# Performance work log

Measured on AMD Instinct MI355X. Metric: run time of the kernel, lower is better.

The kernel has to match this reference:

```python
import jax, jax.numpy as jnp
import numpy as np
import math

B, T, C = 4, 2048, 1024
NH = 16
HD = C // NH


def setup_inputs() -> dict:
    key = jax.random.key(0)
    ks = jax.random.split(key, 10)
    s = 0.02
    x = jax.random.normal(ks[0], (B, T, C), dtype=jnp.float32)
    W_qkv = jax.random.normal(ks[1], (C, 3 * C), dtype=jnp.float32) * s
    b_qkv = jnp.zeros((3 * C,), dtype=jnp.float32)
    W_proj = jax.random.normal(ks[2], (C, C), dtype=jnp.float32) * s
    b_proj = jnp.zeros((C,), dtype=jnp.float32)
    asym_mean, asym_std = 1.0, 0.7
    q_scale = jax.random.normal(ks[3], (NH, HD), dtype=jnp.float32) * asym_std + asym_mean
    q_bias = jax.random.normal(ks[4], (NH, HD), dtype=jnp.float32) * asym_std + asym_mean
    k_scale = jax.random.normal(ks[5], (NH, HD), dtype=jnp.float32) * asym_std + asym_mean
    k_bias = jax.random.normal(ks[6], (NH, HD), dtype=jnp.float32) * asym_std + asym_mean
    return {"x": x, "W_qkv": W_qkv, "b_qkv": b_qkv, "W_proj": W_proj,
            "b_proj": b_proj, "q_scale": q_scale, "q_bias": q_bias,
            "k_scale": k_scale, "k_bias": k_bias}


def reference(x, W_qkv, b_qkv, W_proj, b_proj, q_scale, q_bias, k_scale, k_bias):
    Bx, Tx, Cx = x.shape
    qkv = x @ W_qkv + b_qkv                       # [B,T,3C]
    q, k, v = jnp.split(qkv, 3, axis=-1)
    # [B,T,C] -> [B,NH,T,HD]
    reshape = lambda t: t.reshape(Bx, Tx, NH, HD).transpose(0, 2, 1, 3)
    q, k, v = reshape(q), reshape(k), reshape(v)
    # per-head affine scaling of Q/K
    q = q * q_scale[None, :, None, :] + q_bias[None, :, None, :]
    k = k * k_scale[None, :, None, :] + k_bias[None, :, None, :]
    scores = jnp.einsum('bhqd,bhkd->bhqk', q, k) / math.sqrt(HD)  # [B,NH,T,T]
    causal = jnp.tril(jnp.ones((Tx, Tx), dtype=bool))
    scores = jnp.where(causal[None, None], scores, -jnp.inf)
    att = jax.nn.softmax(scores, axis=-1)
    y = jnp.einsum('bhqk,bhkd->bhqd', att, v)     # [B,NH,T,HD]
    y = y.transpose(0, 2, 1, 3).reshape(Bx, Tx, Cx)
    return y @ W_proj + b_proj
```

## Files before the change

kernel.cpp:

```cpp
#include <hip/hip_runtime.h>
#include <hip/hip_bf16.h>

typedef unsigned short u16;
typedef __attribute__((ext_vector_type(8))) short short8;
typedef __attribute__((ext_vector_type(4))) float floatx4;

#define B_SZ 4
#define T_SZ 2048
#define C_SZ 1024
#define NH_SZ 16
#define HD_SZ 64
#define M_TOT 8192
#define K_DIM 1024

#define QSCALE 0.1803368801111204f

#define OFF_XB   ((size_t)16)
#define OFF_WQT  (OFF_XB + 8388608)
#define OFF_WPT  (OFF_WQT + 3145728)
#define OFF_PB   (OFF_WPT + 1048576)
#define OFF_Q    (OFF_PB + 8192)
#define OFF_K    (OFF_Q + 8388608)
#define OFF_V    (OFF_K + 8388608)
#define OFF_Y    (OFF_V + 8388608)
#define PB_BQKV  0
#define PB_BPROJ 3072
#define PB_QSC   4096
#define PB_QBI   5120
#define PB_KSC   6144
#define PB_KBI   7168

__device__ __forceinline__ float bf2f(u16 u) {
    return __uint_as_float(((unsigned)u) << 16);
}
__device__ __forceinline__ u16 f2bf(float f) {
    unsigned x = __float_as_uint(f);
    unsigned r = (x + 0x7fffu + ((x >> 16) & 1u)) >> 16;
    return (u16)r;
}
__device__ __forceinline__ u16 f2bf_fast(float f) {
    return (u16)((__float_as_uint(f) + 0x8000u) >> 16);
}
__device__ __forceinline__ void gl_lds16(const u16* g, u16* l) {
    __builtin_amdgcn_global_load_lds(
        (const __attribute__((address_space(1))) void*)g,
        (__attribute__((address_space(3))) void*)l, 16, 0, 0);
}
__device__ __forceinline__ int detect_isf(const u16* xx, int lane) {
    float v0 = fabsf(bf2f(xx[lane * 2]));
    float v1 = fabsf(bf2f(xx[lane * 2 + 1]));
    int b0 = (v0 > 1024.0f) || (v0 != 0.0f && v0 < 9.5367431640625e-7f);
    int b1 = (v1 > 1024.0f) || (v1 != 0.0f && v1 < 9.5367431640625e-7f);
    unsigned long long ba = __ballot(b0), bb = __ballot(b1);
    return (__popcll(ba) + __popcll(bb)) > 8;
}

__global__ __launch_bounds__(256) void prep_k(
        const void* __restrict__ x,
        const void* __restrict__ Wqkv, const void* __restrict__ Wproj,
        const void* __restrict__ bqkv, const void* __restrict__ bproj,
        const void* __restrict__ qsc, const void* __restrict__ qbi,
        const void* __restrict__ ksc, const void* __restrict__ kbi,
        u16* __restrict__ xb, u16* __restrict__ Wt_qkv,
        u16* __restrict__ Wt_proj, u16* __restrict__ pb,
        int* __restrict__ flag) {
    __shared__ u16 t[32][33];
    const int blk = blockIdx.x;
    const int isf = detect_isf((const u16*)x, threadIdx.x & 63);
    if (blk == 0 && threadIdx.x == 0) flag[0] = isf;
    if (blk < 8192) {
        const int i = blk * 256 + threadIdx.x;
        if (isf) {
            const float4 v = ((const float4*)x)[i];
            ushort4 o;
            o.x = f2bf(v.x); o.y = f2bf(v.y); o.z = f2bf(v.z); o.w = f2bf(v.w);
            ((ushort4*)xb)[i] = o;
        } else {
            ((ushort4*)xb)[i] = ((const ushort4*)x)[i];
        }
        return;
    }
    if (blk < 8200) {
        const int i4 = (blk - 8192) * 256 + threadIdx.x;
        if (i4 >= 2048) return;
        const int e = i4 * 4;
        const void* src; int off;
        if (e < 3072)      { src = bqkv;  off = e; }
        else if (e < 4096) { src = bproj; off = e - 3072; }
        else if (e < 5120) { src = qsc;   off = e - 4096; }
        else if (e < 6144) { src = qbi;   off = e - 5120; }
        else if (e < 7168) { src = ksc;   off = e - 6144; }
        else               { src = kbi;   off = e - 7168; }
        ushort4 o;
        if (isf) {
            const float4 v = *(const float4*)((const float*)src + off);
            o.x = f2bf(v.x); o.y = f2bf(v.y); o.z = f2bf(v.z); o.w = f2bf(v.w);
        } else {
            o = *(const ushort4*)((const u16*)src + off);
        }
        *(ushort4*)&pb[e] = o;
        return;
    }
    const void* in; u16* out; int R, C, idx;
    if (blk < 11272) { idx = blk - 8200;  in = Wqkv;  out = Wt_qkv;  R = 1024; C = 3072; }
    else             { idx = blk - 11272; in = Wproj; out = Wt_proj; R = 1024; C = 1024; }
    const int nbx = C >> 5;
    const int c0 = (idx % nbx) * 32, r0 = (idx / nbx) * 32;
    const int tx = threadIdx.x & 31, ty = threadIdx.x >> 5;
    for (int i = 0; i < 4; i++) {
        int r = ty + i * 8;
        size_t gi = (size_t)(r0 + r) * C + c0 + tx;
        t[r][tx] = isf ? f2bf(((const float*)in)[gi]) : ((const u16*)in)[gi];
    }
    __syncthreads();
    for (int i = 0; i < 4; i++) {
        int cr = ty + i * 8;
        out[(size_t)(c0 + cr) * R + r0 + tx] = t[tx][cr];
    }
}

#define QG_BM 256
#define QG_BN 192
#define QG_NT 16

__global__ __launch_bounds__(512, 2) void qkv_gemm(
        const u16* __restrict__ X, const u16* __restrict__ Wt,
        const u16* __restrict__ pb,
        u16* __restrict__ Qb, u16* __restrict__ Kb, u16* __restrict__ Vb) {
    __shared__ __align__(16) u16 As[2][QG_BM * 64];
    __shared__ __align__(16) u16 Bs[2][QG_BN * 64];
    const int bm = blockIdx.y * QG_BM, bn = blockIdx.x * QG_BN;
    const int tid = threadIdx.x;
    const int lane = tid & 63, w = tid >> 6;
    const int quad = lane >> 4, l16 = lane & 15;
    const int wm = (w >> 2) * 128;
    const int wn = (w & 3) * 48;
    const int lrow = lane >> 3;
    const int lcol = ((lane & 7) ^ lrow) * 8;
    const int sl0 = ((0 + quad) ^ (l16 & 7)) * 8;
    const int sl1 = ((4 + quad) ^ (l16 & 7)) * 8;

#define QG_STAGE(slot, kt) do {                                                  \
        const int k0_ = (kt) * 64;                                               \
        _Pragma("unroll")                                                        \
        for (int j = 0; j < 4; j++) {                                            \
            const int rb = w * 32 + j * 8;                                       \
            gl_lds16(&X[(size_t)(bm + rb + lrow) * K_DIM + k0_ + lcol],          \
                     &As[slot][rb * 64]);                                        \
        }                                                                        \
        _Pragma("unroll")                                                        \
        for (int j = 0; j < 3; j++) {                                            \
            const int rb = w * 24 + j * 8;                                       \
            gl_lds16(&Wt[(size_t)(bn + rb + lrow) * K_DIM + k0_ + lcol],         \
                     &Bs[slot][rb * 64]);                                        \
        }                                                                        \
    } while (0)

    floatx4 acc[8][3];
#pragma unroll
    for (int mi = 0; mi < 8; mi++)
#pragma unroll
        for (int ni = 0; ni < 3; ni++) acc[mi][ni] = 0.f;

    QG_STAGE(0, 0);
    QG_STAGE(1, 1);
    asm volatile("s_waitcnt vmcnt(7)" ::: "memory");
    __builtin_amdgcn_s_barrier();

    for (int t = 0; t < QG_NT; ++t) {
        const int cur = t & 1;
        const u16* as = As[cur];
        const u16* bs = Bs[cur];
        short8 a[8], b[3];
#pragma unroll
        for (int mi = 0; mi < 8; mi++)
            a[mi] = *(const short8*)&as[(wm + mi * 16 + l16) * 64 + sl0];
#pragma unroll
        for (int ni = 0; ni < 3; ni++)
            b[ni] = *(const short8*)&bs[(wn + ni * 16 + l16) * 64 + sl0];
        __builtin_amdgcn_s_setprio(1);
#pragma unroll
        for (int mi = 0; mi < 8; mi++)
#pragma unroll
            for (int ni = 0; ni < 3; ni++)
                acc[mi][ni] = __builtin_amdgcn_mfma_f32_16x16x32_bf16(
                    a[mi], b[ni], acc[mi][ni], 0, 0, 0);
        __builtin_amdgcn_s_setprio(0);
#pragma unroll
        for (int mi = 0; mi < 8; mi++)
            a[mi] = *(const short8*)&as[(wm + mi * 16 + l16) * 64 + sl1];
#pragma unroll
        for (int ni = 0; ni < 3; ni++)
            b[ni] = *(const short8*)&bs[(wn + ni * 16 + l16) * 64 + sl1];
        asm volatile("s_waitcnt lgkmcnt(0)" ::: "memory");
        __builtin_amdgcn_s_barrier();
        if (t < QG_NT - 1) {
            const int tn = (t + 2 < QG_NT) ? t + 2 : QG_NT - 1;
            QG_STAGE(cur, tn);
        }
        __builtin_amdgcn_s_setprio(1);
#pragma unroll
        for (int mi = 0; mi < 8; mi++)
#pragma unroll
            for (int ni = 0; ni < 3; ni++)
                acc[mi][ni] = __builtin_amdgcn_mfma_f32_16x16x32_bf16(
                    a[mi], b[ni], acc[mi][ni], 0, 0, 0);
        __builtin_amdgcn_s_setprio(0);
        asm volatile("s_waitcnt vmcnt(7)" ::: "memory");
        __builtin_amdgcn_s_barrier();
    }
#undef QG_STAGE

    const int bb = bm >> 11;
    const int tbase = bm & 2047;
#pragma unroll
    for (int ni = 0; ni < 3; ni++) {
        const int col = bn + wn + ni * 16 + l16;
        const int sec = col >> 10;
        const int cmod = col & 1023;
        const int h = cmod >> 6, d = cmod & 63;
        const float bv = bf2f(pb[PB_BQKV + col]);
        if (sec == 2) {
#pragma unroll
            for (int mi = 0; mi < 8; mi++) {
                const int t0 = tbase + wm + mi * 16 + quad * 4;
                ushort4 pk;
                pk.x = f2bf(acc[mi][ni][0] + bv);
                pk.y = f2bf(acc[mi][ni][1] + bv);
                pk.z = f2bf(acc[mi][ni][2] + bv);
                pk.w = f2bf(acc[mi][ni][3] + bv);
                *(ushort4*)&Vb[(((size_t)(bb * NH_SZ + h)) * HD_SZ + d) * T_SZ + t0] = pk;
            }
        } else {
            float sA, sB;
            if (sec == 0) {
                sA = bf2f(pb[PB_QSC + h * 64 + d]) * QSCALE;
                sB = bf2f(pb[PB_QBI + h * 64 + d]) * QSCALE;
            } else {
                sA = bf2f(pb[PB_KSC + h * 64 + d]);
                sB = bf2f(pb[PB_KBI + h * 64 + d]);
            }
            u16* dstbuf = (sec == 0) ? Qb : Kb;
#pragma unroll
            for (int mi = 0; mi < 8; mi++)
#pragma unroll
                for (int r = 0; r < 4; r++) {
                    const int tt = tbase + wm + mi * 16 + quad * 4 + r;
                    float v = (acc[mi][ni][r] + bv) * sA + sB;
                    dstbuf[(((size_t)(bb * NH_SZ + h)) * T_SZ + tt) * HD_SZ + d] = f2bf(v);
                }
        }
    }
}

__global__ __launch_bounds__(512) void attn_k(const u16* __restrict__ Qb,
                                              const u16* __restrict__ Kb,
                                              const u16* __restrict__ Vtg,
                                              u16* __restrict__ Y) {
    __shared__ __align__(16) u16 Ks[64 * 64];
    __shared__ __align__(16) u16 Vs[64 * 64];
    __shared__ __align__(16) u16 Ps[8 * 16 * 88];
    const int blk = blockIdx.x;
    const int head = blk & 63;
    const int p = blk >> 6;
    const int b = head >> 4, h = head & 15;
    const int tid = threadIdx.x, lane = tid & 63, w = tid >> 6;
    const int quad = lane >> 4, l16 = lane & 15;
    const size_t qk_off = (size_t)head * (T_SZ * HD_SZ);
    const size_t v_off = (size_t)head * (HD_SZ * T_SZ);
    u16* psw = &Ps[w * 1408];
    const int lr = lane >> 3;
    const int lc = ((lane & 7) ^ lr) * 8;
    const int sl0 = ((quad) ^ (l16 & 7)) * 8;
    const int sl1 = ((4 + quad) ^ (l16 & 7)) * 8;

    short8 ones;
    for (int j = 0; j < 8; j++) ones[j] = (short)0x3F80;

    for (int tile = 0; tile < 2; tile++) {
        const int qt = tile ? p : (15 - p);
        const int q0 = qt * 128;
        const int rbase = q0 + w * 16;
        const int q = rbase + l16;

        const short8 aq0 = *(const short8*)&Qb[qk_off + (size_t)q * HD_SZ + quad * 8];
        const short8 aq1 = *(const short8*)&Qb[qk_off + (size_t)q * HD_SZ + 32 + quad * 8];

        floatx4 o[4];
        for (int mi = 0; mi < 4; mi++) o[mi] = 0.f;
        float m_run = -1e30f, l_run = 0.f;

        for (int k0 = 0; k0 < q0 + 128; k0 += 64) {
            __syncthreads();
            gl_lds16(&Kb[qk_off + (size_t)(k0 + w * 8 + lr) * HD_SZ + lc], &Ks[w * 512]);
            gl_lds16(&Vtg[v_off + (size_t)(w * 8 + lr) * T_SZ + k0 + lc], &Vs[w * 512]);
            __syncthreads();
            if (k0 > rbase + 15) continue;

            floatx4 s[4];
            for (int ni = 0; ni < 4; ni++) s[ni] = 0.f;
            for (int ni = 0; ni < 4; ni++)
                s[ni] = __builtin_amdgcn_mfma_f32_16x16x32_bf16(
                    *(const short8*)&Ks[(ni * 16 + l16) * 64 + sl0], aq0, s[ni], 0, 0, 0);
            for (int ni = 0; ni < 4; ni++)
                s[ni] = __builtin_amdgcn_mfma_f32_16x16x32_bf16(
                    *(const short8*)&Ks[(ni * 16 + l16) * 64 + sl1], aq1, s[ni], 0, 0, 0);

            if (k0 + 63 > rbase) {
                for (int ni = 0; ni < 4; ni++)
                    for (int r = 0; r < 4; r++) {
                        int key = k0 + ni * 16 + quad * 4 + r;
                        if (key > q) s[ni][r] = -1e30f;
                    }
            }

            float mx = fmaxf(fmaxf(s[0][0], s[0][1]), fmaxf(s[0][2], s[0][3]));
            for (int ni = 1; ni < 4; ni++)
                mx = fmaxf(mx, fmaxf(fmaxf(s[ni][0], s[ni][1]),
                                     fmaxf(s[ni][2], s[ni][3])));
            mx = fmaxf(mx, __shfl_xor(mx, 16, 64));
            mx = fmaxf(mx, __shfl_xor(mx, 32, 64));
            const float mnew = fmaxf(m_run, mx);
            const float alpha = exp2f(m_run - mnew);
            for (int ni = 0; ni < 4; ni++)
                for (int r = 0; r < 4; r++)
                    s[ni][r] = exp2f(s[ni][r] - mnew);
            m_run = mnew;
            for (int mi = 0; mi < 4; mi++) o[mi] *= alpha;

            for (int ni = 0; ni < 4; ni++) {
                ushort4 pk;
                pk.x = f2bf_fast(s[ni][0]); pk.y = f2bf_fast(s[ni][1]);
                pk.z = f2bf_fast(s[ni][2]); pk.w = f2bf_fast(s[ni][3]);
                *(ushort4*)&psw[l16 * 88 + ni * 16 + quad * 4] = pk;
            }

            floatx4 s4 = 0.f;
            for (int kk = 0; kk < 64; kk += 32) {
                short8 pfr = *(const short8*)&psw[l16 * 88 + kk + quad * 8];
                const int vsl = (kk == 0) ? sl0 : sl1;
                s4 = __builtin_amdgcn_mfma_f32_16x16x32_bf16(ones, pfr, s4, 0, 0, 0);
                for (int mi = 0; mi < 4; mi++) {
                    short8 vfr = *(const short8*)&Vs[(mi * 16 + l16) * 64 + vsl];
                    o[mi] = __builtin_amdgcn_mfma_f32_16x16x32_bf16(vfr, pfr, o[mi], 0, 0, 0);
                }
            }
            l_run = l_run * alpha + s4[0];
        }

        const float inv = 1.0f / l_run;
        u16* yrow = &Y[(((size_t)b * T_SZ + q) * NH_SZ + h) * HD_SZ];
        for (int mi = 0; mi < 4; mi++) {
            ushort4 pk;
            pk.x = f2bf_fast(o[mi][0] * inv); pk.y = f2bf_fast(o[mi][1] * inv);
            pk.z = f2bf_fast(o[mi][2] * inv); pk.w = f2bf_fast(o[mi][3] * inv);
            *(ushort4*)&yrow[mi * 16 + quad * 4] = pk;
        }
    }
}

__global__ __launch_bounds__(256) void proj_gemm(const u16* __restrict__ Yin,
                                                 const u16* __restrict__ Wt,
                                                 const u16* __restrict__ pb,
                                                 void* __restrict__ out,
                                                 const int* __restrict__ flag) {
    __shared__ __align__(16) u16 As[128 * 64];
    __shared__ __align__(16) u16 Bs[128 * 64];
    const int isf = flag[0];
    const int bm = blockIdx.y * 128, bn = blockIdx.x * 128;
    const int tid = threadIdx.x;
    const int lane = tid & 63, wave = tid >> 6;
    const int quad = lane >> 4, l16 = lane & 15;
    const int wm = (wave & 1) * 64, wn = (wave >> 1) * 64;
    const int lrow = lane >> 3;
    const int lcol = ((lane & 7) ^ lrow) * 8;

    floatx4 acc[4][4];
    for (int mi = 0; mi < 4; mi++)
        for (int ni = 0; ni < 4; ni++) acc[mi][ni] = 0.f;

    for (int k0 = 0; k0 < K_DIM; k0 += 64) {
        __syncthreads();
        for (int j = 0; j < 4; j++) {
            const int rb = wave * 32 + j * 8;
            gl_lds16(&Yin[(size_t)(bm + rb + lrow) * K_DIM + k0 + lcol], &As[rb * 64]);
            gl_lds16(&Wt[(size_t)(bn + rb + lrow) * K_DIM + k0 + lcol], &Bs[rb * 64]);
        }
        __syncthreads();
        for (int kk = 0; kk < 64; kk += 32) {
            const int cb = kk >> 3;
            const int slot = ((cb + quad) ^ (l16 & 7)) * 8;
            short8 a[4], b[4];
            for (int mi = 0; mi < 4; mi++)
                a[mi] = *(const short8*)&As[(wm + mi * 16 + l16) * 64 + slot];
            for (int ni = 0; ni < 4; ni++)
                b[ni] = *(const short8*)&Bs[(wn + ni * 16 + l16) * 64 + slot];
            for (int mi = 0; mi < 4; mi++)
                for (int ni = 0; ni < 4; ni++)
                    acc[mi][ni] = __builtin_amdgcn_mfma_f32_16x16x32_bf16(
                        a[mi], b[ni], acc[mi][ni], 0, 0, 0);
        }
    }

    for (int mi = 0; mi < 4; mi++) {
        for (int ni = 0; ni < 4; ni++) {
            const int col = bn + wn + ni * 16 + l16;
            const float bv = bf2f(pb[PB_BPROJ + col]);
            for (int r = 0; r < 4; r++) {
                const int row = bm + wm + mi * 16 + quad * 4 + r;
                const float v = acc[mi][ni][r] + bv;
                if (isf) ((float*)out)[(size_t)row * C_SZ + col] = v;
                else     ((u16*)out)[(size_t)row * C_SZ + col] = f2bf(v);
            }
        }
    }
}

extern "C" void kernel_launch(void* const* d_in, const int* in_sizes, int n_in,
                              void* d_out, int out_size, void* d_ws, size_t ws_size,
                              hipStream_t stream) {
    const void* x     = d_in[0];
    const void* Wqkv  = d_in[1];
    const void* bqkv  = d_in[2];
    const void* Wproj = d_in[3];
    const void* bproj = d_in[4];
    const void* qsc   = d_in[5];
    const void* qbi   = d_in[6];
    const void* ksc   = d_in[7];
    const void* kbi   = d_in[8];

    u16* ws = (u16*)d_ws;
    int* flag    = (int*)d_ws;
    u16* xb      = ws + OFF_XB;
    u16* Wt_qkv  = ws + OFF_WQT;
    u16* Wt_proj = ws + OFF_WPT;
    u16* pb      = ws + OFF_PB;
    u16* Qb      = ws + OFF_Q;
    u16* Kb      = ws + OFF_K;
    u16* Vb      = ws + OFF_V;
    u16* Yb      = ws + OFF_Y;

    prep_k<<<12296, 256, 0, stream>>>(x, Wqkv, Wproj, bqkv, bproj,
                                      qsc, qbi, ksc, kbi,
                                      xb, Wt_qkv, Wt_proj, pb, flag);
    qkv_gemm<<<dim3(16, 32), 512, 0, stream>>>(xb, Wt_qkv, pb, Qb, Kb, Vb);
    attn_k<<<dim3(512), 512, 0, stream>>>(Qb, Kb, Vb, Yb);
    proj_gemm<<<dim3(8, 64), 256, 0, stream>>>(Yb, Wt_proj, pb, d_out, flag);
}
```

Baseline: 297.5 us.

## Double-buffer K/V and projection GEMM tiles with async loads, lazy softmax rescale

Attention now double-buffers the K/V tiles in LDS. The next tile's global-to-LDS load is issued before computing on the current one, using explicit vmcnt waits and barriers instead of two __syncthreads per step. The online softmax skips rescaling of the output and running sum unless the running max grows by more than 8 (in log2 units), and packs bf16 with v_cvt_pk_bf16_f32. The projection GEMM gets a two-stage LDS pipeline that prefetches k-tile t+2 while computing, plus s_setprio around MFMA bursts and launch bounds of 2 blocks per SM. The costs are doubled LDS use, which may lower occupancy, and more fragile hand-written waitcnt logic; the lazy rescale lets unnormalised exponentials grow up to 2^8.

```diff
diff --git a/kernel.cpp b/kernel.cpp
--- a/kernel.cpp
+++ b/kernel.cpp
@@ -40,6 +40,11 @@
 }
 __device__ __forceinline__ u16 f2bf_fast(float f) {
     return (u16)((__float_as_uint(f) + 0x8000u) >> 16);
+}
+__device__ __forceinline__ unsigned cvt_pk_bf16(float lo, float hi) {
+    unsigned r;
+    asm("v_cvt_pk_bf16_f32 %0, %1, %2" : "=v"(r) : "v"(lo), "v"(hi));
+    return r;
 }
 __device__ __forceinline__ void gl_lds16(const u16* g, u16* l) {
     __builtin_amdgcn_global_load_lds(
@@ -257,8 +262,8 @@
                                               const u16* __restrict__ Kb,
                                               const u16* __restrict__ Vtg,
                                               u16* __restrict__ Y) {
-    __shared__ __align__(16) u16 Ks[64 * 64];
-    __shared__ __align__(16) u16 Vs[64 * 64];
+    __shared__ __align__(16) u16 Ks[2][64 * 64];
+    __shared__ __align__(16) u16 Vs[2][64 * 64];
     __shared__ __align__(16) u16 Ps[8 * 16 * 88];
     const int blk = blockIdx.x;
     const int head = blk & 63;
@@ -282,6 +287,7 @@
         const int q0 = qt * 128;
         const int rbase = q0 + w * 16;
         const int q = rbase + l16;
+        const int nt = (q0 >> 6) + 2;
 
         const short8 aq0 = *(const short8*)&Qb[qk_off + (size_t)q * HD_SZ + quad * 8];
         const short8 aq1 = *(const short8*)&Qb[qk_off + (size_t)q * HD_SZ + 32 + quad * 8];
@@ -290,117 +296,185 @@
         for (int mi = 0; mi < 4; mi++) o[mi] = 0.f;
         float m_run = -1e30f, l_run = 0.f;
 
-        for (int k0 = 0; k0 < q0 + 128; k0 += 64) {
-            __syncthreads();
-            gl_lds16(&Kb[qk_off + (size_t)(k0 + w * 8 + lr) * HD_SZ + lc], &Ks[w * 512]);
-            gl_lds16(&Vtg[v_off + (size_t)(w * 8 + lr) * T_SZ + k0 + lc], &Vs[w * 512]);
-            __syncthreads();
-            if (k0 > rbase + 15) continue;
-
-            floatx4 s[4];
-            for (int ni = 0; ni < 4; ni++) s[ni] = 0.f;
-            for (int ni = 0; ni < 4; ni++)
-                s[ni] = __builtin_amdgcn_mfma_f32_16x16x32_bf16(
-                    *(const short8*)&Ks[(ni * 16 + l16) * 64 + sl0], aq0, s[ni], 0, 0, 0);
-            for (int ni = 0; ni < 4; ni++)
-                s[ni] = __builtin_amdgcn_mfma_f32_16x16x32_bf16(
-                    *(const short8*)&Ks[(ni * 16 + l16) * 64 + sl1], aq1, s[ni], 0, 0, 0);
-
-            if (k0 + 63 > rbase) {
+        gl_lds16(&Kb[qk_off + (size_t)(w * 8 + lr) * HD_SZ + lc], &Ks[0][w * 512]);
+        gl_lds16(&Vtg[v_off + (size_t)(w * 8 + lr) * T_SZ + lc], &Vs[0][w * 512]);
+
+        for (int t = 0; t < nt; ++t) {
+            const int cur = t & 1;
+            const int k0 = t * 64;
+            if (t + 1 < nt) {
+                const int kn = k0 + 64;
+                gl_lds16(&Kb[qk_off + (size_t)(kn + w * 8 + lr) * HD_SZ + lc],
+                         &Ks[cur ^ 1][w * 512]);
+                gl_lds16(&Vtg[v_off + (size_t)(w * 8 + lr) * T_SZ + kn + lc],
+                         &Vs[cur ^ 1][w * 512]);
+                asm volatile("s_waitcnt vmcnt(2)" ::: "memory");
+            } else {
+                asm volatile("s_waitcnt vmcnt(0)" ::: "memory");
+            }
+            __builtin_amdgcn_s_barrier();
+
+            if (k0 <= rbase + 15) {
+                const u16* ks = Ks[cur];
+                const u16* vs = Vs[cur];
+                floatx4 s[4];
+                for (int ni = 0; ni < 4; ni++) s[ni] = 0.f;
                 for (int ni = 0; ni < 4; ni++)
-                    for (int r = 0; r < 4; r++) {
-                        int key = k0 + ni * 16 + quad * 4 + r;
-                        if (key > q) s[ni][r] = -1e30f;
+                    s[ni] = __builtin_amdgcn_mfma_f32_16x16x32_bf16(
+                        *(const short8*)&ks[(ni * 16 + l16) * 64 + sl0], aq0, s[ni], 0, 0, 0);
+                for (int ni = 0; ni < 4; ni++)
+                    s[ni] = __builtin_amdgcn_mfma_f32_16x16x32_bf16(
+                        *(const short8*)&ks[(ni * 16 + l16) * 64 + sl1], aq1, s[ni], 0, 0, 0);
+
+                if (k0 + 63 > rbase) {
+                    for (int ni = 0; ni < 4; ni++)
+                        for (int r = 0; r < 4; r++) {
+                            int key = k0 + ni * 16 + quad * 4 + r;
+                            if (key > q) s[ni][r] = -1e30f;
+                        }
+                }
+
+                float t0 = fmaxf(fmaxf(s[0][0], s[0][1]), s[0][2]);
+                float t1 = fmaxf(fmaxf(s[0][3], s[1][0]), s[1][1]);
+                float t2 = fmaxf(fmaxf(s[1][2], s[1][3]), s[2][0]);
+                float t3 = fmaxf(fmaxf(s[2][1], s[2][2]), s[2][3]);
+                float t4 = fmaxf(fmaxf(s[3][0], s[3][1]), s[3][2]);
+                float mx = fmaxf(fmaxf(fmaxf(t0, t1), fmaxf(t2, t3)),
+                                 fmaxf(t4, s[3][3]));
+                mx = fmaxf(mx, __shfl_xor(mx, 16, 64));
+                mx = fmaxf(mx, __shfl_xor(mx, 32, 64));
+
+                if (!__all(mx <= m_run + 8.0f)) {
+                    const float mnew = fmaxf(m_run, mx);
+                    const float alpha = exp2f(m_run - mnew);
+                    m_run = mnew;
+                    for (int mi = 0; mi < 4; mi++) o[mi] *= alpha;
+                    l_run *= alpha;
+                }
+                for (int ni = 0; ni < 4; ni++)
+                    for (int r = 0; r < 4; r++)
+                        s[ni][r] = exp2f(s[ni][r] - m_run);
+
+                for (int ni = 0; ni < 4; ni++) {
+                    uint2 pp;
+                    pp.x = cvt_pk_bf16(s[ni][0], s[ni][1]);
+                    pp.y = cvt_pk_bf16(s[ni][2], s[ni][3]);
+                    *(uint2*)&psw[l16 * 88 + ni * 16 + quad * 4] = pp;
+                }
+
+                floatx4 s4 = 0.f;
+                for (int kk = 0; kk < 64; kk += 32) {
+                    short8 pfr = *(const short8*)&psw[l16 * 88 + kk + quad * 8];
+                    const int vsl = (kk == 0) ? sl0 : sl1;
+                    s4 = __builtin_amdgcn_mfma_f32_16x16x32_bf16(ones, pfr, s4, 0, 0, 0);
+                    for (int mi = 0; mi < 4; mi++) {
+                        short8 vfr = *(const short8*)&vs[(mi * 16 + l16) * 64 + vsl];
+                        o[mi] = __builtin_amdgcn_mfma_f32_16x16x32_bf16(vfr, pfr, o[mi], 0, 0, 0);
                     }
+                }
+                l_run += s4[0];
             }
-
-            float mx = fmaxf(fmaxf(s[0][0], s[0][1]), fmaxf(s[0][2], s[0][3]));
-            for (int ni = 1; ni < 4; ni++)
-                mx = fmaxf(mx, fmaxf(fmaxf(s[ni][0], s[ni][1]),
-                                     fmaxf(s[ni][2], s[ni][3])));
-            mx = fmaxf(mx, __shfl_xor(mx, 16, 64));
-            mx = fmaxf(mx, __shfl_xor(mx, 32, 64));
-            const float mnew = fmaxf(m_run, mx);
-            const float alpha = exp2f(m_run - mnew);
-            for (int ni = 0; ni < 4; ni++)
-                for (int r = 0; r < 4; r++)
-                    s[ni][r] = exp2f(s[ni][r] - mnew);
-            m_run = mnew;
-            for (int mi = 0; mi < 4; mi++) o[mi] *= alpha;
-
-            for (int ni = 0; ni < 4; ni++) {
-                ushort4 pk;
-                pk.x = f2bf_fast(s[ni][0]); pk.y = f2bf_fast(s[ni][1]);
-                pk.z = f2bf_fast(s[ni][2]); pk.w = f2bf_fast(s[ni][3]);
-                *(ushort4*)&psw[l16 * 88 + ni * 16 + quad * 4] = pk;
-            }
-
-            floatx4 s4 = 0.f;
-            for (int kk = 0; kk < 64; kk += 32) {
-                short8 pfr = *(const short8*)&psw[l16 * 88 + kk + quad * 8];
-                const int vsl = (kk == 0) ? sl0 : sl1;
-                s4 = __builtin_amdgcn_mfma_f32_16x16x32_bf16(ones, pfr, s4, 0, 0, 0);
-                for (int mi = 0; mi < 4; mi++) {
-                    short8 vfr = *(const short8*)&Vs[(mi * 16 + l16) * 64 + vsl];
-                    o[mi] = __builtin_amdgcn_mfma_f32_16x16x32_bf16(vfr, pfr, o[mi], 0, 0, 0);
-                }
-            }
-            l_run = l_run * alpha + s4[0];
+            asm volatile("s_waitcnt lgkmcnt(0)" ::: "memory");
+            __builtin_amdgcn_s_barrier();
         }
 
         const float inv = 1.0f / l_run;
         u16* yrow = &Y[(((size_t)b * T_SZ + q) * NH_SZ + h) * HD_SZ];
         for (int mi = 0; mi < 4; mi++) {
-            ushort4 pk;
-            pk.x = f2bf_fast(o[mi][0] * inv); pk.y = f2bf_fast(o[mi][1] * inv);
-            pk.z = f2bf_fast(o[mi][2] * inv); pk.w = f2bf_fast(o[mi][3] * inv);
-            *(ushort4*)&yrow[mi * 16 + quad * 4] = pk;
-        }
-    }
-}
-
-__global__ __launch_bounds__(256) void proj_gemm(const u16* __restrict__ Yin,
-                                                 const u16* __restrict__ Wt,
-                                                 const u16* __restrict__ pb,
-                                                 void* __restrict__ out,
-                                                 const int* __restrict__ flag) {
-    __shared__ __align__(16) u16 As[128 * 64];
-    __shared__ __align__(16) u16 Bs[128 * 64];
+            uint2 pk2;
+            pk2.x = cvt_pk_bf16(o[mi][0] * inv, o[mi][1] * inv);
+            pk2.y = cvt_pk_bf16(o[mi][2] * inv, o[mi][3] * inv);
+            *(uint2*)&yrow[mi * 16 + quad * 4] = pk2;
+        }
+    }
+}
+
+#define PG_NT 16
+
+__global__ __launch_bounds__(256, 2) void proj_gemm(const u16* __restrict__ Yin,
+                                                    const u16* __restrict__ Wt,
+                                                    const u16* __restrict__ pb,
+                                                    void* __restrict__ out,
+                                                    const int* __restrict__ flag) {
+    __shared__ __align__(16) u16 As[2][128 * 64];
+    __shared__ __align__(16) u16 Bs[2][128 * 64];
     const int isf = flag[0];
     const int bm = blockIdx.y * 128, bn = blockIdx.x * 128;
     const int tid = threadIdx.x;
-    const int lane = tid & 63, wave = tid >> 6;
+    const int lane = tid & 63, w = tid >> 6;
     const int quad = lane >> 4, l16 = lane & 15;
-    const int wm = (wave & 1) * 64, wn = (wave >> 1) * 64;
+    const int wm = (w & 1) * 64, wn = (w >> 1) * 64;
     const int lrow = lane >> 3;
     const int lcol = ((lane & 7) ^ lrow) * 8;
+    const int sl0 = ((0 + quad) ^ (l16 & 7)) * 8;
+    const int sl1 = ((4 + quad) ^ (l16 & 7)) * 8;
+
+#define PG_STAGE(slot, kt) do {                                                  \
+        const int k0_ = (kt) * 64;                                               \
+        _Pragma("unroll")                                                        \
+        for (int j = 0; j < 4; j++) {                                            \
+            const int rb = w * 32 + j * 8;                                       \
+            gl_lds16(&Yin[(size_t)(bm + rb + lrow) * K_DIM + k0_ + lcol],        \
+                     &As[slot][rb * 64]);                                        \
+            gl_lds16(&Wt[(size_t)(bn + rb + lrow) * K_DIM + k0_ + lcol],         \
+                     &Bs[slot][rb * 64]);                                        \
+        }                                                                        \
+    } while (0)
 
     floatx4 acc[4][4];
+#pragma unroll
     for (int mi = 0; mi < 4; mi++)
+#pragma unroll
         for (int ni = 0; ni < 4; ni++) acc[mi][ni] = 0.f;
 
-    for (int k0 = 0; k0 < K_DIM; k0 += 64) {
-        __syncthreads();
-        for (int j = 0; j < 4; j++) {
-            const int rb = wave * 32 + j * 8;
-            gl_lds16(&Yin[(size_t)(bm + rb + lrow) * K_DIM + k0 + lcol], &As[rb * 64]);
-            gl_lds16(&Wt[(size_t)(bn + rb + lrow) * K_DIM + k0 + lcol], &Bs[rb * 64]);
-        }
-        __syncthreads();
-        for (int kk = 0; kk < 64; kk += 32) {
-            const int cb = kk >> 3;
-            const int slot = ((cb + quad) ^ (l16 & 7)) * 8;
-            short8 a[4], b[4];
-            for (int mi = 0; mi < 4; mi++)
-                a[mi] = *(const short8*)&As[(wm + mi * 16 + l16) * 64 + slot];
+    PG_STAGE(0, 0);
+    PG_STAGE(1, 1);
+    asm volatile("s_waitcnt vmcnt(8)" ::: "memory");
+    __builtin_amdgcn_s_barrier();
+
+    for (int t = 0; t < PG_NT; ++t) {
+        const int cur = t & 1;
+        const u16* as = As[cur];
+        const u16* bs = Bs[cur];
+        short8 a[4], b[4];
+#pragma unroll
+        for (int mi = 0; mi < 4; mi++)
+            a[mi] = *(const short8*)&as[(wm + mi * 16 + l16) * 64 + sl0];
+#pragma unroll
+        for (int ni = 0; ni < 4; ni++)
+            b[ni] = *(const short8*)&bs[(wn + ni * 16 + l16) * 64 + sl0];
+        __builtin_amdgcn_s_setprio(1);
+#pragma unroll
+        for (int mi = 0; mi < 4; mi++)
+#pragma unroll
             for (int ni = 0; ni < 4; ni++)
-                b[ni] = *(const short8*)&Bs[(wn + ni * 16 + l16) * 64 + slot];
-            for (int mi = 0; mi < 4; mi++)
-                for (int ni = 0; ni < 4; ni++)
-                    acc[mi][ni] = __builtin_amdgcn_mfma_f32_16x16x32_bf16(
-                        a[mi], b[ni], acc[mi][ni], 0, 0, 0);
-        }
-    }
+                acc[mi][ni] = __builtin_amdgcn_mfma_f32_16x16x32_bf16(
+                    a[mi], b[ni], acc[mi][ni], 0, 0, 0);
+        __builtin_amdgcn_s_setprio(0);
+#pragma unroll
+        for (int mi = 0; mi < 4; mi++)
+            a[mi] = *(const short8*)&as[(wm + mi * 16 + l16) * 64 + sl1];
+#pragma unroll
+        for (int ni = 0; ni < 4; ni++)
+            b[ni] = *(const short8*)&bs[(wn + ni * 16 + l16) * 64 + sl1];
+        asm volatile("s_waitcnt lgkmcnt(0)" ::: "memory");
+        __builtin_amdgcn_s_barrier();
+        if (t < PG_NT - 1) {
+            const int tn = (t + 2 < PG_NT) ? t + 2 : PG_NT - 1;
+            PG_STAGE(cur, tn);
+        }
+        __builtin_amdgcn_s_setprio(1);
+#pragma unroll
+        for (int mi = 0; mi < 4; mi++)
+#pragma unroll
+            for (int ni = 0; ni < 4; ni++)
+                acc[mi][ni] = __builtin_amdgcn_mfma_f32_16x16x32_bf16(
+                    a[mi], b[ni], acc[mi][ni], 0, 0, 0);
+        __builtin_amdgcn_s_setprio(0);
+        asm volatile("s_waitcnt vmcnt(8)" ::: "memory");
+        __builtin_amdgcn_s_barrier();
+    }
+#undef PG_STAGE
 
     for (int mi = 0; mi < 4; mi++) {
         for (int ni = 0; ni < 4; ni++) {
```

Measured after the change: 283.5 us. 4.7% less time.
